# Kernel tuning notes

Hardware: AMD Instinct MI355X
Metric: run time of the kernel (lower is better)

The kernel has to match this reference:

```python
import jax, jax.numpy as jnp
import numpy as np

DIM = 256
HEADS = 8
HD = DIM // HEADS
SR = 2
SCALE = HD ** -0.5
EPS = 1e-5


def _layernorm(t, g, b):
    m = jnp.mean(t, axis=-1, keepdims=True)
    v = jnp.mean((t - m) ** 2, axis=-1, keepdims=True)
    return (t - m) / jnp.sqrt(v + EPS) * g + b


def _sr_kv(t, H, W, sr_w, sr_b, ln_g, ln_b, Wkv):
    # t: [B, N, C] with N == H*W -> spatial-reduction conv -> LN -> kv proj
    B, N, C = t.shape
    img = t.transpose(0, 2, 1).reshape(B, C, H, W)
    red = jax.lax.conv_general_dilated(
        img, sr_w, window_strides=(SR, SR), padding='VALID',
        dimension_numbers=('NCHW', 'OIHW', 'NCHW')) + sr_b[None, :, None, None]
    red = red.reshape(B, C, -1).transpose(0, 2, 1)  # [B, Nr, C]
    red = _layernorm(red, ln_g, ln_b)
    Nr = red.shape[1]
    kv = (red @ Wkv).reshape(B, Nr, 2, HEADS, HD).transpose(2, 0, 3, 1, 4)
    return kv[0], kv[1]  # k, v: [B, h, Nr, d]


def _q_heads(t, Wq):
    B, N, _ = t.shape
    return (t @ Wq).reshape(B, N, HEADS, HD).transpose(0, 2, 1, 3)  # [B,h,N,d]


def _attn_out(q, k, v, proj_w, proj_b):
    a = jnp.einsum('bhqd,bhkd->bhqk', q, k) * SCALE
    a = jax.nn.softmax(a, axis=-1)
    o = jnp.einsum('bhqk,bhkd->bhqd', a, v)
    B, h, N, d = o.shape
    return o.transpose(0, 2, 1, 3).reshape(B, N, h * d) @ proj_w + proj_b


def _forward(x, y, Wq, Wkv, sr_w, sr_b, ln_g, ln_b, proj_w, proj_b,
             H_x, W_x, H_y, W_y):
    # B_x == 1 branch of the original module (static shapes)
    B_y = y.shape[0]
    q_x = _q_heads(x, Wq)
    q_y = _q_heads(y, Wq)
    k_x, v_x = _sr_kv(x, H_x, W_x, sr_w, sr_b, ln_g, ln_b, Wkv)
    k_y, v_y = _sr_kv(y, H_y, W_y, sr_w, sr_b, ln_g, ln_b, Wkv)
    # x attends to its own KV + batch-averaged support KV
    k_cat_x = jnp.concatenate([k_x, jnp.mean(k_y, axis=0, keepdims=True)], axis=2)
    v_cat_x = jnp.concatenate([v_x, jnp.mean(v_y, axis=0, keepdims=True)], axis=2)
    x_out = _attn_out(q_x, k_cat_x, v_cat_x, proj_w, proj_b)
    # each support attends to repeated query KV + its own KV
    k_cat_y = jnp.concatenate([jnp.broadcast_to(k_x, (B_y,) + k_x.shape[1:]), k_y], axis=2)
    v_cat_y = jnp.concatenate([jnp.broadcast_to(v_x, (B_y,) + v_x.shape[1:]), v_y], axis=2)
    y_out = _attn_out(q_y, k_cat_y, v_cat_y, proj_w, proj_b)
    return x_out, y_out


def setup_inputs() -> dict:
    key = jax.random.key(0)
    ks = jax.random.split(key, 6)
    std = 0.02
    return {
        'x': jax.random.normal(ks[0], (1, 6400, DIM), jnp.float32),
        'y': jax.random.normal(ks[1], (4, 1024, DIM), jnp.float32),
        'Wq': jax.random.normal(ks[2], (DIM, DIM), jnp.float32) * std,
        'Wkv': jax.random.normal(ks[3], (DIM, 2 * DIM), jnp.float32) * std,
        'sr_w': jax.random.normal(ks[4], (DIM, DIM, SR, SR), jnp.float32) * np.sqrt(2.0 / (SR * SR * DIM)),
        'sr_b': jnp.zeros((DIM,), jnp.float32),
        'ln_g': jnp.ones((DIM,), jnp.float32),
        'ln_b': jnp.zeros((DIM,), jnp.float32),
        'proj_w': jax.random.normal(ks[5], (DIM, DIM), jnp.float32) * std,
        'proj_b': jnp.zeros((DIM,), jnp.float32),
        'H_x': 80, 'W_x': 80, 'H_y': 32, 'W_y': 32,
    }


def reference(x, y, Wq, Wkv, sr_w, sr_b, ln_g, ln_b, proj_w, proj_b,
              H_x, W_x, H_y, W_y):
    return _forward(x, y, Wq, Wkv, sr_w, sr_b, ln_g, ln_b, proj_w, proj_b,
                    H_x, W_x, H_y, W_y)
```

## Files before the change

kernel.cpp:

```cpp
#include <hip/hip_runtime.h>
#include <math.h>

#define DIM 256
#define HD 32
#define KSCALE (0.17677669529663687f * 1.44269504088896340736f)
#define EPS 1e-5f

typedef __attribute__((ext_vector_type(8))) short short8;
typedef __attribute__((ext_vector_type(4))) float f32x4;

__device__ inline unsigned short f2bf(float f) {
    union { float f; unsigned u; } v; v.f = f;
    unsigned r = v.u + 0x7FFF + ((v.u >> 16) & 1);
    return (unsigned short)(r >> 16);
}
__device__ inline float bf2f(unsigned short h) {
    union { unsigned u; float f; } v; v.u = ((unsigned)h) << 16;
    return v.f;
}
__device__ inline unsigned pk2bf(float a, float b) {
    unsigned ua = __float_as_uint(a) + 0x8000u;
    unsigned ub = __float_as_uint(b) + 0x8000u;
    return __builtin_amdgcn_perm(ub, ua, 0x07060302u);
}
__device__ inline uint4 pk8bf(float4 a, float4 b) {
    return make_uint4(pk2bf(a.x, a.y), pk2bf(a.z, a.w),
                      pk2bf(b.x, b.y), pk2bf(b.z, b.w));
}
__device__ inline void up2(unsigned u, float& a, float& b) {
    a = __uint_as_float(u << 16);
    b = __uint_as_float(u & 0xffff0000u);
}
#define MFMA16(a, b, c) __builtin_amdgcn_mfma_f32_16x16x32_bf16(a, b, c, 0, 0, 0)
#define EXP2(x) __builtin_amdgcn_exp2f(x)

__global__ __launch_bounds__(256) void prep_w(
    const float* __restrict__ Wq, const float* __restrict__ Wkv,
    const float* __restrict__ projw, const float* __restrict__ srw,
    unsigned short* __restrict__ WqT, unsigned short* __restrict__ WkvT,
    unsigned short* __restrict__ projT, unsigned short* __restrict__ BwT)
{
    int idx = blockIdx.x * 256 + threadIdx.x;
    if (idx < 65536) { int n = idx >> 8, k = idx & 255; WqT[idx] = f2bf(Wq[(k << 8) + n]); return; }
    idx -= 65536;
    if (idx < 131072) { int n = idx >> 8, k = idx & 255; WkvT[idx] = f2bf(Wkv[(k << 9) + n]); return; }
    idx -= 131072;
    if (idx < 65536) { int n = idx >> 8, k = idx & 255; projT[idx] = f2bf(projw[(k << 8) + n]); return; }
    idx -= 65536;
    { int o = idx >> 10, rem = idx & 1023, q = rem >> 8, i = rem & 255;
      BwT[idx] = f2bf(srw[(o << 10) + (i << 2) + q]); }
}

__global__ __launch_bounds__(256) void convq_kernel(
    const float* __restrict__ x, const float* __restrict__ y,
    const unsigned short* __restrict__ BwT, const float* __restrict__ srb,
    const unsigned short* __restrict__ WqT,
    unsigned short* __restrict__ redx, unsigned short* __restrict__ redy,
    unsigned short* __restrict__ qxb, unsigned short* __restrict__ qyb)
{
    __shared__ __align__(16) unsigned short At[64][32];
    __shared__ __align__(16) unsigned short Btile[64][32];
    const int tid = threadIdx.x;
    const int lane = tid & 63, w = tid >> 6;
    const int c = lane & 15, quad = lane >> 4;
    const int srow = tid >> 2, sch = (tid & 3) << 3;
    const int bid = blockIdx.x;
    f32x4 acc[4] = {};
    const int rl = (w << 4) + (quad << 2);

    if (bid < 164) {
        const int n0 = (bid & 3) << 6, myi = bid >> 2;
        const float* Xb; unsigned short* Cb; int W, W2, m0;
        if (myi < 25) { Xb = x; Cb = redx; W = 80; W2 = 40; m0 = myi * 64; }
        else {
            const int r = myi - 25, b = r >> 2;
            Xb = y + (size_t)b * 262144; Cb = redy + (size_t)b * 65536;
            W = 32; W2 = 16; m0 = (r & 3) * 64;
        }
        const int p = m0 + srow;
        const int oy = p / W2, ox = p - oy * W2;
        const unsigned short* Bp = BwT + (size_t)(n0 + srow) * 1024 + sch;

        auto addrA = [&](int k0) {
            const int qq = k0 >> 8;
            const int rrow = (2 * oy + (qq >> 1)) * W + 2 * ox + (qq & 1);
            return Xb + (size_t)rrow * DIM + (k0 & 255) + sch;
        };

        const float* ap = addrA(0);
        float4 a0 = *(const float4*)ap, a1 = *(const float4*)(ap + 4);
        uint4 bn = *(const uint4*)Bp;
        for (int k0 = 0; k0 < 1024; k0 += 32) {
            *(uint4*)&At[srow][sch]    = pk8bf(a0, a1);
            *(uint4*)&Btile[srow][sch] = bn;
            if (k0 < 992) {
                const float* np = addrA(k0 + 32);
                a0 = *(const float4*)np; a1 = *(const float4*)(np + 4);
                bn = *(const uint4*)(Bp + k0 + 32);
            }
            __syncthreads();
            short8 a = *(short8*)&At[(w << 4) + c][quad << 3];
            #pragma unroll
            for (int nb = 0; nb < 4; ++nb) {
                short8 b = *(short8*)&Btile[(nb << 4) + c][quad << 3];
                acc[nb] = MFMA16(a, b, acc[nb]);
            }
            __syncthreads();
        }
        #pragma unroll
        for (int nb = 0; nb < 4; ++nb) {
            const int col = n0 + (nb << 4) + c;
            const float bv = srb[col];
            #pragma unroll
            for (int r = 0; r < 4; ++r)
                Cb[(size_t)(m0 + rl + r) * DIM + col] = f2bf(acc[nb][r] + bv);
        }
    } else {
        const int r = bid - 164;
        const int n0 = (r & 3) << 6, mg = (r >> 2) << 6;
        const float* Ab = (mg < 6400) ? x + (size_t)mg * 256
                                      : y + (size_t)(mg - 6400) * 256;
        unsigned short* Cb = (mg < 6400) ? qxb + (size_t)mg * 256
                                         : qyb + (size_t)(mg - 6400) * 256;
        const float* Ap = Ab + (size_t)srow * 256 + sch;
        const unsigned short* Bp = WqT + (size_t)(n0 + srow) * 256 + sch;

        float4 a0 = *(const float4*)Ap, a1 = *(const float4*)(Ap + 4);
        uint4 bn = *(const uint4*)Bp;
        for (int k0 = 0; k0 < 256; k0 += 32) {
            *(uint4*)&At[srow][sch]    = pk8bf(a0, a1);
            *(uint4*)&Btile[srow][sch] = bn;
            if (k0 < 224) {
                a0 = *(const float4*)(Ap + k0 + 32);
                a1 = *(const float4*)(Ap + k0 + 36);
                bn = *(const uint4*)(Bp + k0 + 32);
            }
            __syncthreads();
            short8 a = *(short8*)&At[(w << 4) + c][quad << 3];
            #pragma unroll
            for (int nb = 0; nb < 4; ++nb) {
                short8 b = *(short8*)&Btile[(nb << 4) + c][quad << 3];
                acc[nb] = MFMA16(a, b, acc[nb]);
            }
            __syncthreads();
        }
        #pragma unroll
        for (int nb = 0; nb < 4; ++nb) {
            const int col = n0 + (nb << 4) + c;
            #pragma unroll
            for (int r = 0; r < 4; ++r)
                Cb[(size_t)(rl + r) * 256 + col] = f2bf(acc[nb][r]);
        }
    }
}

__global__ __launch_bounds__(256) void kvln_kernel(
    const unsigned short* __restrict__ redx, const unsigned short* __restrict__ redy,
    const unsigned short* __restrict__ WkvT,
    const float* __restrict__ g, const float* __restrict__ bta,
    unsigned short* __restrict__ kbx, unsigned short* __restrict__ vTx,
    unsigned short* __restrict__ kby, unsigned short* __restrict__ vTy)
{
    __shared__ __align__(16) unsigned short At[64][32];
    __shared__ __align__(16) unsigned short Btile[64][32];
    const int tid = threadIdx.x;
    const int lane = tid & 63, w = tid >> 6;
    const int c = lane & 15, quad = lane >> 4;
    const int srow = tid >> 2, sch = (tid & 3) << 3;
    const int bid = blockIdx.x;
    const int n0 = (bid & 7) << 6, mg = (bid >> 3) << 6;
    const unsigned short* Ab = (mg < 1600) ? redx + (size_t)mg * 256
                                           : redy + (size_t)(mg - 1600) * 256;
    const unsigned short* Arow = Ab + (size_t)srow * 256 + sch;

    uint4 araw[8];
    float s1 = 0.f, s2 = 0.f;
    #pragma unroll
    for (int ci = 0; ci < 8; ++ci) {
        araw[ci] = *(const uint4*)(Arow + (ci << 5));
        const unsigned* du = (const unsigned*)&araw[ci];
        #pragma unroll
        for (int dd = 0; dd < 4; ++dd) {
            float a, b; up2(du[dd], a, b);
            s1 += a + b; s2 += a * a + b * b;
        }
    }
    s1 += __shfl_xor(s1, 1); s1 += __shfl_xor(s1, 2);
    s2 += __shfl_xor(s2, 1); s2 += __shfl_xor(s2, 2);
    const float mean = s1 * (1.0f / 256.0f);
    const float var  = s2 * (1.0f / 256.0f) - mean * mean;
    const float rstd = rsqrtf(var + EPS);

    #pragma unroll
    for (int ci = 0; ci < 8; ++ci) {
        const int ch = (ci << 5) + sch;
        float4 g0 = *(const float4*)(g + ch),   g1 = *(const float4*)(g + ch + 4);
        float4 b0 = *(const float4*)(bta + ch), b1 = *(const float4*)(bta + ch + 4);
        const unsigned* du = (const unsigned*)&araw[ci];
        float v[8];
        #pragma unroll
        for (int dd = 0; dd < 4; ++dd) up2(du[dd], v[2 * dd], v[2 * dd + 1]);
        float4 o0 = make_float4(fmaf((v[0] - mean) * rstd, g0.x, b0.x),
                                fmaf((v[1] - mean) * rstd, g0.y, b0.y),
                                fmaf((v[2] - mean) * rstd, g0.z, b0.z),
                                fmaf((v[3] - mean) * rstd, g0.w, b0.w));
        float4 o1 = make_float4(fmaf((v[4] - mean) * rstd, g1.x, b1.x),
                                fmaf((v[5] - mean) * rstd, g1.y, b1.y),
                                fmaf((v[6] - mean) * rstd, g1.z, b1.z),
                                fmaf((v[7] - mean) * rstd, g1.w, b1.w));
        araw[ci] = pk8bf(o0, o1);
    }

    const unsigned short* Bp = WkvT + (size_t)(n0 + srow) * 256 + sch;
    uint4 bn = *(const uint4*)Bp;
    f32x4 acc[4] = {};
    for (int k0 = 0; k0 < 256; k0 += 32) {
        *(uint4*)&At[srow][sch]    = araw[k0 >> 5];
        *(uint4*)&Btile[srow][sch] = bn;
        if (k0 < 224) bn = *(const uint4*)(Bp + k0 + 32);
        __syncthreads();
        short8 a = *(short8*)&At[(w << 4) + c][quad << 3];
        #pragma unroll
        for (int nb = 0; nb < 4; ++nb) {
            short8 b = *(short8*)&Btile[(nb << 4) + c][quad << 3];
            acc[nb] = MFMA16(a, b, acc[nb]);
        }
        __syncthreads();
    }

    const int rl = (w << 4) + (quad << 2);
    #pragma unroll
    for (int nb = 0; nb < 4; ++nb) {
        const int col = n0 + (nb << 4) + c;
        if (col < 256) {
            unsigned short* Cb = (mg < 1600) ? kbx + (size_t)mg * 256
                                             : kby + (size_t)(mg - 1600) * 256;
            #pragma unroll
            for (int r = 0; r < 4; ++r)
                Cb[(size_t)(rl + r) * 256 + col] = f2bf(acc[nb][r] * KSCALE);
        } else {
            unsigned lo = (unsigned)f2bf(acc[nb][0]) | ((unsigned)f2bf(acc[nb][1]) << 16);
            unsigned hi = (unsigned)f2bf(acc[nb][2]) | ((unsigned)f2bf(acc[nb][3]) << 16);
            unsigned short* Vb = (mg < 1600)
                ? vTx + (size_t)(col - 256) * 1600 + mg
                : vTy + (size_t)(col - 256) * 1024 + (mg - 1600);
            *(uint2*)(Vb + rl) = make_uint2(lo, hi);
        }
    }
}

__global__ __launch_bounds__(256) void kvmean_kernel(
    const unsigned short* __restrict__ kby, const unsigned short* __restrict__ vTy,
    unsigned short* __restrict__ km, unsigned short* __restrict__ vmT)
{
    int idx = blockIdx.x * 256 + threadIdx.x;
    if (idx < 65536) {
        float s = bf2f(kby[idx]) + bf2f(kby[idx + 65536]) +
                  bf2f(kby[idx + 131072]) + bf2f(kby[idx + 196608]);
        km[idx] = f2bf(0.25f * s);
    } else {
        int e = idx - 65536; int hd = e >> 8, r = e & 255;
        const unsigned short* p = vTy + ((size_t)hd << 10);
        float s = bf2f(p[r]) + bf2f(p[r + 256]) + bf2f(p[r + 512]) + bf2f(p[r + 768]);
        vmT[((size_t)hd << 8) + r] = f2bf(0.25f * s);
    }
}

__global__ __launch_bounds__(256) void attn_mfma(
    unsigned short* __restrict__ qxb, unsigned short* __restrict__ qyb,
    const unsigned short* __restrict__ kbx, const unsigned short* __restrict__ vTx,
    const unsigned short* __restrict__ km,  const unsigned short* __restrict__ vmT,
    const unsigned short* __restrict__ kby, const unsigned short* __restrict__ vTy)
{
    __shared__ __align__(16) unsigned short Pt[64][72];
    __shared__ __align__(16) float lpart[64][17];
    __shared__ __align__(16) float lsum[64];

    const int tid = threadIdx.x;
    const int lane = tid & 63, w = tid >> 6;
    const int c = lane & 15, quad = lane >> 4;
    const int dch = w & 1;
    const int qb2 = (w >> 1) << 1;

    const int bid = blockIdx.x;
    unsigned short* qb; const unsigned short *kb2, *vT2;
    int h, qoff, R2;
    if (bid < 800) {
        h = bid / 100; qoff = (bid - h * 100) * 64;
        qb = qxb; kb2 = km; vT2 = vmT; R2 = 256;
    } else {
        const int idx = bid - 800, b = idx >> 7, rem = idx & 127;
        h = rem >> 4; qoff = b * 1024 + (rem & 15) * 64;
        qb = qyb; kb2 = kby + (size_t)b * 65536; vT2 = vTy + b * 256; R2 = 1024;
    }

    short8 qf[4];
    #pragma unroll
    for (int nb = 0; nb < 4; ++nb)
        qf[nb] = *(const short8*)(qb + (size_t)(qoff + (nb << 4) + c) * DIM + h * HD + (quad << 3));

    const int kOff = ((w << 4) + c) * DIM + h * HD + (quad << 3);
    const int vRow = h * HD + (dch << 4) + c;
    const unsigned short* k1p = kbx + kOff;
    const unsigned short* k2p = kb2 + kOff;
    const unsigned short* v1p = vTx + (size_t)vRow * 1600 + (quad << 3);
    const unsigned short* v2p = vT2 + (size_t)vRow * R2 + (quad << 3);

    auto ldKV = [&](int t, short8& ka, short8& v0, short8& v1) {
        const unsigned short *kp, *vp;
        if (t < 25) { kp = k1p + (t << 14); vp = v1p + (t << 6); }
        else        { kp = k2p + ((t - 25) << 14); vp = v2p + ((t - 25) << 6); }
        ka = *(const short8*)kp;
        v0 = *(const short8*)vp;
        v1 = *(const short8*)(vp + 32);
    };

    float lsr[4] = {0.f, 0.f, 0.f, 0.f};
    f32x4 oacc[2] = {};
    const f32x4 zero = {0.f, 0.f, 0.f, 0.f};

    short8 kaA, v0A, v1A, kaB, v0B, v1B;
    ldKV(0, kaA, v0A, v1A);
    ldKV(1, kaB, v0B, v1B);

    auto body = [&](int t, short8& ka, short8& v0, short8& v1) {
        f32x4 sacc[4];
        #pragma unroll
        for (int nb = 0; nb < 4; ++nb) sacc[nb] = MFMA16(ka, qf[nb], zero);
        #pragma unroll
        for (int nb = 0; nb < 4; ++nb) {
            float p0 = EXP2(sacc[nb][0]);
            float p1 = EXP2(sacc[nb][1]);
            float p2 = EXP2(sacc[nb][2]);
            float p3 = EXP2(sacc[nb][3]);
            lsr[nb] += (p0 + p1) + (p2 + p3);
            *(uint2*)&Pt[(nb << 4) + c][(w << 4) + (quad << 2)] =
                make_uint2(pk2bf(p0, p1), pk2bf(p2, p3));
        }
        __syncthreads();
        #pragma unroll
        for (int q2 = 0; q2 < 2; ++q2) {
            short8 pf0 = *(short8*)&Pt[((qb2 + q2) << 4) + c][(quad << 3)];
            short8 pf1 = *(short8*)&Pt[((qb2 + q2) << 4) + c][32 + (quad << 3)];
            oacc[q2] = MFMA16(pf0, v0, oacc[q2]);
            oacc[q2] = MFMA16(pf1, v1, oacc[q2]);
        }
        if (t + 2 < 29) ldKV(t + 2, ka, v0, v1);
        __syncthreads();
    };

    for (int t = 0; t < 29; t += 2) {
        body(t, kaA, v0A, v1A);
        if (t + 1 < 29) body(t + 1, kaB, v0B, v1B);
    }

    #pragma unroll
    for (int nb = 0; nb < 4; ++nb)
        lpart[(nb << 4) + c][(w << 2) + quad] = lsr[nb];
    __syncthreads();
    if (tid < 64) {
        float s = 0.f;
        #pragma unroll
        for (int i = 0; i < 16; ++i) s += lpart[tid][i];
        lsum[tid] = s;
    }
    __syncthreads();

    #pragma unroll
    for (int q2 = 0; q2 < 2; ++q2) {
        const int rowb = ((qb2 + q2) << 4) + (quad << 2);
        #pragma unroll
        for (int r = 0; r < 4; ++r) {
            const float inv = 1.0f / lsum[rowb + r];
            qb[(size_t)(qoff + rowb + r) * DIM + h * HD + (dch << 4) + c] =
                f2bf(oacc[q2][r] * inv);
        }
    }
}

__global__ __launch_bounds__(256) void proj_mfma(
    const unsigned short* __restrict__ qxb, const unsigned short* __restrict__ qyb,
    const unsigned short* __restrict__ projT, const float* __restrict__ bias,
    float* __restrict__ outx, float* __restrict__ outy)
{
    __shared__ __align__(16) unsigned short At[64][32];
    __shared__ __align__(16) unsigned short Btile[64][32];
    const int tid = threadIdx.x;
    const int lane = tid & 63, w = tid >> 6;
    const int c = lane & 15, quad = lane >> 4;
    const int srow = tid >> 2, sch = (tid & 3) << 3;

    const int bid = blockIdx.x;
    const int n0 = (bid & 3) << 6, mg = (bid >> 2) << 6;
    const unsigned short* Ab = (mg < 6400) ? qxb + (size_t)mg * 256
                                           : qyb + (size_t)(mg - 6400) * 256;
    float* Cf = (mg < 6400) ? outx + (size_t)mg * 256 : outy + (size_t)(mg - 6400) * 256;

    const unsigned short* Ap = Ab + (size_t)srow * 256 + sch;
    const unsigned short* Bp = projT + (size_t)(n0 + srow) * 256 + sch;

    uint4 an = *(const uint4*)Ap, bn = *(const uint4*)Bp;
    f32x4 acc[4] = {};
    for (int k0 = 0; k0 < 256; k0 += 32) {
        *(uint4*)&At[srow][sch]    = an;
        *(uint4*)&Btile[srow][sch] = bn;
        if (k0 < 224) { an = *(const uint4*)(Ap + k0 + 32); bn = *(const uint4*)(Bp + k0 + 32); }
        __syncthreads();
        short8 a = *(short8*)&At[(w << 4) + c][quad << 3];
        #pragma unroll
        for (int nb = 0; nb < 4; ++nb) {
            short8 b = *(short8*)&Btile[(nb << 4) + c][quad << 3];
            acc[nb] = MFMA16(a, b, acc[nb]);
        }
        __syncthreads();
    }
    const int rl = (w << 4) + (quad << 2);
    #pragma unroll
    for (int nb = 0; nb < 4; ++nb) {
        const int col = n0 + (nb << 4) + c;
        const float bv = bias[col];
        #pragma unroll
        for (int r = 0; r < 4; ++r)
            Cf[(size_t)(rl + r) * 256 + col] = acc[nb][r] + bv;
    }
}

extern "C" void kernel_launch(void* const* d_in, const int* in_sizes, int n_in,
                              void* d_out, int out_size, void* d_ws, size_t ws_size,
                              hipStream_t stream)
{
    const float* x      = (const float*)d_in[0];
    const float* y      = (const float*)d_in[1];
    const float* Wq     = (const float*)d_in[2];
    const float* Wkv    = (const float*)d_in[3];
    const float* sr_w   = (const float*)d_in[4];
    const float* sr_b   = (const float*)d_in[5];
    const float* ln_g   = (const float*)d_in[6];
    const float* ln_b   = (const float*)d_in[7];
    const float* proj_w = (const float*)d_in[8];
    const float* proj_b = (const float*)d_in[9];

    unsigned short* p = (unsigned short*)d_ws;
    unsigned short* WqT   = p;  p += 65536;
    unsigned short* WkvT  = p;  p += 131072;
    unsigned short* projT = p;  p += 65536;
    unsigned short* BwT   = p;  p += 262144;
    unsigned short* redx  = p;  p += 409600;
    unsigned short* redy  = p;  p += 262144;
    unsigned short* qxb   = p;  p += 1638400;
    unsigned short* qyb   = p;  p += 1048576;
    unsigned short* kbx   = p;  p += 409600;
    unsigned short* vTx   = p;  p += 409600;
    unsigned short* kby   = p;  p += 262144;
    unsigned short* vTy   = p;  p += 262144;
    unsigned short* km    = p;  p += 65536;
    unsigned short* vmT   = p;  p += 65536;
    float* outx = (float*)d_out;
    float* outy = outx + 6400 * 256;

    prep_w<<<2048, 256, 0, stream>>>(Wq, Wkv, proj_w, sr_w, WqT, WkvT, projT, BwT);
    convq_kernel<<<820, 256, 0, stream>>>(x, y, BwT, sr_b, WqT, redx, redy, qxb, qyb);
    kvln_kernel<<<328, 256, 0, stream>>>(redx, redy, WkvT, ln_g, ln_b,
                                         kbx, vTx, kby, vTy);
    kvmean_kernel<<<512, 256, 0, stream>>>(kby, vTy, km, vmT);
    attn_mfma<<<1312, 256, 0, stream>>>(qxb, qyb, kbx, vTx, km, vmT, kby, vTy);
    proj_mfma<<<656, 256, 0, stream>>>(qxb, qyb, projT, proj_b, outx, outy);
}
```

Baseline: 189.8 us.

## Keep attention probabilities in registers by permuting V layout to match MFMA output

The attention kernel now gives each wave its own 16 query rows and loops over all 64 keys per tile itself. The QK^T MFMA output is packed directly into the A operand of the PV MFMA, so the shared-memory P tile and both per-tile block barriers are removed. To make the register layouts line up, the KV projection kernel writes transposed V with a permuted key order (tau), and row sums are reduced with wave shuffles instead of shared memory. Each wave now loads four K fragments and four V fragments per tile, so it issues more global loads and holds more registers.

```diff
diff --git a/kernel.cpp b/kernel.cpp
--- a/kernel.cpp
+++ b/kernel.cpp
@@ -8,6 +8,8 @@
 
 typedef __attribute__((ext_vector_type(8))) short short8;
 typedef __attribute__((ext_vector_type(4))) float f32x4;
+
+union U8 { uint4 u; short8 s; };
 
 __device__ inline unsigned short f2bf(float f) {
     union { float f; unsigned u; } v; v.f = f;
@@ -229,6 +231,7 @@
     }
 
     const int rl = (w << 4) + (quad << 2);
+    const int tau = ((w >> 1) << 5) + (quad << 3) + ((w & 1) << 2);
     #pragma unroll
     for (int nb = 0; nb < 4; ++nb) {
         const int col = n0 + (nb << 4) + c;
@@ -244,7 +247,7 @@
             unsigned short* Vb = (mg < 1600)
                 ? vTx + (size_t)(col - 256) * 1600 + mg
                 : vTy + (size_t)(col - 256) * 1024 + (mg - 1600);
-            *(uint2*)(Vb + rl) = make_uint2(lo, hi);
+            *(uint2*)(Vb + tau) = make_uint2(lo, hi);
         }
     }
 }
@@ -272,15 +275,9 @@
     const unsigned short* __restrict__ km,  const unsigned short* __restrict__ vmT,
     const unsigned short* __restrict__ kby, const unsigned short* __restrict__ vTy)
 {
-    __shared__ __align__(16) unsigned short Pt[64][72];
-    __shared__ __align__(16) float lpart[64][17];
-    __shared__ __align__(16) float lsum[64];
-
     const int tid = threadIdx.x;
     const int lane = tid & 63, w = tid >> 6;
     const int c = lane & 15, quad = lane >> 4;
-    const int dch = w & 1;
-    const int qb2 = (w >> 1) << 1;
 
     const int bid = blockIdx.x;
     unsigned short* qb; const unsigned short *kb2, *vT2;
@@ -291,90 +288,79 @@
     } else {
         const int idx = bid - 800, b = idx >> 7, rem = idx & 127;
         h = rem >> 4; qoff = b * 1024 + (rem & 15) * 64;
-        qb = qyb; kb2 = kby + (size_t)b * 65536; vT2 = vTy + b * 256; R2 = 1024;
-    }
-
-    short8 qf[4];
-    #pragma unroll
-    for (int nb = 0; nb < 4; ++nb)
-        qf[nb] = *(const short8*)(qb + (size_t)(qoff + (nb << 4) + c) * DIM + h * HD + (quad << 3));
-
-    const int kOff = ((w << 4) + c) * DIM + h * HD + (quad << 3);
-    const int vRow = h * HD + (dch << 4) + c;
-    const unsigned short* k1p = kbx + kOff;
-    const unsigned short* k2p = kb2 + kOff;
-    const unsigned short* v1p = vTx + (size_t)vRow * 1600 + (quad << 3);
-    const unsigned short* v2p = vT2 + (size_t)vRow * R2 + (quad << 3);
-
-    auto ldKV = [&](int t, short8& ka, short8& v0, short8& v1) {
-        const unsigned short *kp, *vp;
-        if (t < 25) { kp = k1p + (t << 14); vp = v1p + (t << 6); }
-        else        { kp = k2p + ((t - 25) << 14); vp = v2p + ((t - 25) << 6); }
-        ka = *(const short8*)kp;
-        v0 = *(const short8*)vp;
-        v1 = *(const short8*)(vp + 32);
+        qb = qyb; kb2 = kby + (size_t)b * 65536; vT2 = vTy + b * 256;
+        R2 = 1024;
+    }
+
+    const int qrow = qoff + (w << 4) + c;
+    const short8 qf = *(const short8*)(qb + (size_t)qrow * DIM + h * HD + (quad << 3));
+
+    const unsigned short* k1 = kbx + (size_t)c * DIM + h * HD + (quad << 3);
+    const unsigned short* k2 = kb2 + (size_t)c * DIM + h * HD + (quad << 3);
+    const unsigned short* v1b0 = vTx + (size_t)(h * HD + c) * 1600 + (quad << 3);
+    const unsigned short* v1b1 = vTx + (size_t)(h * HD + 16 + c) * 1600 + (quad << 3);
+    const unsigned short* v2b0 = vT2 + (size_t)(h * HD + c) * R2 + (quad << 3);
+    const unsigned short* v2b1 = vT2 + (size_t)(h * HD + 16 + c) * R2 + (quad << 3);
+
+    auto ld = [&](int t, short8* ka, short8* va) {
+        const unsigned short* kp;
+        const unsigned short *vb0, *vb1; int off;
+        if (t < 25) { kp = k1 + ((size_t)t << 14); off = t << 6; vb0 = v1b0; vb1 = v1b1; }
+        else { kp = k2 + ((size_t)(t - 25) << 14); off = (t - 25) << 6; vb0 = v2b0; vb1 = v2b1; }
+        #pragma unroll
+        for (int kb = 0; kb < 4; ++kb) ka[kb] = *(const short8*)(kp + (kb << 12));
+        va[0] = *(const short8*)(vb0 + off);
+        va[1] = *(const short8*)(vb1 + off);
+        va[2] = *(const short8*)(vb0 + off + 32);
+        va[3] = *(const short8*)(vb1 + off + 32);
     };
 
-    float lsr[4] = {0.f, 0.f, 0.f, 0.f};
+    float lsr = 0.f;
     f32x4 oacc[2] = {};
     const f32x4 zero = {0.f, 0.f, 0.f, 0.f};
 
-    short8 kaA, v0A, v1A, kaB, v0B, v1B;
-    ldKV(0, kaA, v0A, v1A);
-    ldKV(1, kaB, v0B, v1B);
-
-    auto body = [&](int t, short8& ka, short8& v0, short8& v1) {
+    short8 kaA[4], vaA[4], kaB[4], vaB[4];
+    ld(0, kaA, vaA);
+
+    auto body = [&](int t, short8* ka, short8* va, short8* kan, short8* van) {
         f32x4 sacc[4];
         #pragma unroll
-        for (int nb = 0; nb < 4; ++nb) sacc[nb] = MFMA16(ka, qf[nb], zero);
-        #pragma unroll
-        for (int nb = 0; nb < 4; ++nb) {
-            float p0 = EXP2(sacc[nb][0]);
-            float p1 = EXP2(sacc[nb][1]);
-            float p2 = EXP2(sacc[nb][2]);
-            float p3 = EXP2(sacc[nb][3]);
-            lsr[nb] += (p0 + p1) + (p2 + p3);
-            *(uint2*)&Pt[(nb << 4) + c][(w << 4) + (quad << 2)] =
-                make_uint2(pk2bf(p0, p1), pk2bf(p2, p3));
-        }
-        __syncthreads();
-        #pragma unroll
-        for (int q2 = 0; q2 < 2; ++q2) {
-            short8 pf0 = *(short8*)&Pt[((qb2 + q2) << 4) + c][(quad << 3)];
-            short8 pf1 = *(short8*)&Pt[((qb2 + q2) << 4) + c][32 + (quad << 3)];
-            oacc[q2] = MFMA16(pf0, v0, oacc[q2]);
-            oacc[q2] = MFMA16(pf1, v1, oacc[q2]);
-        }
-        if (t + 2 < 29) ldKV(t + 2, ka, v0, v1);
-        __syncthreads();
+        for (int kb = 0; kb < 4; ++kb) sacc[kb] = MFMA16(ka[kb], qf, zero);
+        if (t + 1 < 29) ld(t + 1, kan, van);
+        float p[16];
+        #pragma unroll
+        for (int kb = 0; kb < 4; ++kb) {
+            p[4 * kb + 0] = EXP2(sacc[kb][0]);
+            p[4 * kb + 1] = EXP2(sacc[kb][1]);
+            p[4 * kb + 2] = EXP2(sacc[kb][2]);
+            p[4 * kb + 3] = EXP2(sacc[kb][3]);
+            lsr += (p[4 * kb + 0] + p[4 * kb + 1]) + (p[4 * kb + 2] + p[4 * kb + 3]);
+        }
+        U8 af0, af1;
+        af0.u = make_uint4(pk2bf(p[0], p[1]), pk2bf(p[2], p[3]),
+                           pk2bf(p[4], p[5]), pk2bf(p[6], p[7]));
+        af1.u = make_uint4(pk2bf(p[8], p[9]), pk2bf(p[10], p[11]),
+                           pk2bf(p[12], p[13]), pk2bf(p[14], p[15]));
+        oacc[0] = MFMA16(af0.s, va[0], oacc[0]);
+        oacc[1] = MFMA16(af0.s, va[1], oacc[1]);
+        oacc[0] = MFMA16(af1.s, va[2], oacc[0]);
+        oacc[1] = MFMA16(af1.s, va[3], oacc[1]);
     };
 
     for (int t = 0; t < 29; t += 2) {
-        body(t, kaA, v0A, v1A);
-        if (t + 1 < 29) body(t + 1, kaB, v0B, v1B);
-    }
+        body(t, kaA, vaA, kaB, vaB);
+        if (t + 1 < 29) body(t + 1, kaB, vaB, kaA, vaA);
+    }
+
+    lsr += __shfl_xor(lsr, 16);
+    lsr += __shfl_xor(lsr, 32);
 
     #pragma unroll
-    for (int nb = 0; nb < 4; ++nb)
-        lpart[(nb << 4) + c][(w << 2) + quad] = lsr[nb];
-    __syncthreads();
-    if (tid < 64) {
-        float s = 0.f;
-        #pragma unroll
-        for (int i = 0; i < 16; ++i) s += lpart[tid][i];
-        lsum[tid] = s;
-    }
-    __syncthreads();
-
-    #pragma unroll
-    for (int q2 = 0; q2 < 2; ++q2) {
-        const int rowb = ((qb2 + q2) << 4) + (quad << 2);
-        #pragma unroll
-        for (int r = 0; r < 4; ++r) {
-            const float inv = 1.0f / lsum[rowb + r];
-            qb[(size_t)(qoff + rowb + r) * DIM + h * HD + (dch << 4) + c] =
-                f2bf(oacc[q2][r] * inv);
-        }
+    for (int r = 0; r < 4; ++r) {
+        const float inv = 1.0f / __shfl(lsr, (quad << 2) + r);
+        const int row = qoff + (w << 4) + (quad << 2) + r;
+        qb[(size_t)row * DIM + h * HD + c]      = f2bf(oacc[0][r] * inv);
+        qb[(size_t)row * DIM + h * HD + 16 + c] = f2bf(oacc[1][r] * inv);
     }
 }
 
```

After: 276.9 us. 1.46x slower.
